# Kernel tuning notes

Hardware: AMD Instinct MI355X
Metric: run time of the kernel (lower is better)

The kernel has to match this reference:

```python
import jax, jax.numpy as jnp
import numpy as np
from jax import lax

L = 8
PATCH = 3
DIRS = [(0, 1), (1, 0), (1, 1), (1, -1)]


def _pair_indices():
    coords = np.arange(PATCH * PATCH)
    rr, cc = coords // PATCH, coords % PATCH
    i1s, i2s = [], []
    for dr, dc in DIRS:
        m = (rr + dr >= 0) & (rr + dr < PATCH) & (cc + dc >= 0) & (cc + dc < PATCH)
        i1s.append(coords[m])
        i2s.append((rr[m] + dr) * PATCH + (cc[m] + dc))
    return np.concatenate(i1s), np.concatenate(i2s)

_I1, _I2 = _pair_indices()


def conv_bn_silu(x, w, s, b, pad):
    # Conv2d(bias=False) + eval-mode BatchNorm folded into (s, b) + SiLU
    y = lax.conv_general_dilated(x, w, (1, 1), [(pad, pad), (pad, pad)],
                                 dimension_numbers=("NCHW", "OIHW", "NCHW"))
    y = y * s[None, :, None, None] + b[None, :, None, None]
    return jax.nn.silu(y)


def glcm_feats(x):
    B, C, H, W = x.shape
    pad = PATCH // 2
    xp = jnp.pad(x, ((0, 0), (0, 0), (pad, pad), (pad, pad)), mode="edge")
    # unfold: (B, C, 9, H, W)
    patches = jnp.stack([xp[:, :, i:i + H, j:j + W]
                         for i in range(PATCH) for j in range(PATCH)], axis=2)
    q = jnp.clip((patches * (L - 1)).astype(jnp.int32), 0, L - 1)
    q = q.reshape(B * C, PATCH * PATCH, H * W)
    # co-occurrence pair indices for all 4 directions, concatenated: (BC, K, HW)
    idx = q[:, _I1, :] * L + q[:, _I2, :]
    idx = idx.transpose(0, 2, 1)  # (BC, HW, K)
    # per-pixel local histogram over L*L bins (scatter-add)
    hist = jax.vmap(jax.vmap(
        lambda v: jnp.zeros((L * L,), x.dtype).at[v].add(1.0)))(idx)
    hist = hist / len(DIRS)  # reduce_mode='average'
    s = jnp.maximum(hist.sum(-1, keepdims=True), 1e-6)
    p = hist / s  # (BC, HW, L*L)
    li = jnp.arange(L, dtype=x.dtype)
    diff = li[:, None] - li[None, :]
    diff_sq = (diff ** 2).reshape(-1)
    abs_d = jnp.abs(diff).reshape(-1)
    contrast = (p * diff_sq).sum(-1)
    energy = (p * p).sum(-1)
    entropy = -(p * jnp.log(p + 1e-6)).sum(-1)
    homog = (p / (1.0 + abs_d)).sum(-1)
    f = jnp.stack([contrast, energy, entropy, homog], axis=-1)  # (BC, HW, 4)
    f = f.reshape(B, C, H * W, 4).mean(axis=1)  # average over channels
    return f.transpose(0, 2, 1).reshape(B, 4, H, W)


def setup_inputs() -> dict:
    key = jax.random.key(0)
    B, C, H, W = 4, 64, 80, 80
    c_, cb, c2 = 32, 16, 64
    ks = iter(jax.random.split(key, 20))
    x = jax.random.uniform(next(ks), (B, C, H, W), jnp.float32)

    def conv_p(cin, cout, ksz):
        w = jax.random.normal(next(ks), (cout, cin, ksz, ksz), jnp.float32) / np.sqrt(cin * ksz * ksz)
        s = jax.random.uniform(next(ks), (cout,), jnp.float32, 0.5, 1.5)
        b = jax.random.normal(next(ks), (cout,), jnp.float32) * 0.1
        return w, s, b

    cv1_w, cv1_s, cv1_b = conv_p(C + 4, c_, 1)
    cv2_w, cv2_s, cv2_b = conv_p(C + 4, c_, 1)
    m1_w, m1_s, m1_b = conv_p(c_, cb, 1)
    m2_w, m2_s, m2_b = conv_p(cb, c_, 3)
    cv3_w, cv3_s, cv3_b = conv_p(2 * c_, c2, 1)
    return dict(x=x, cv1_w=cv1_w, cv1_s=cv1_s, cv1_b=cv1_b,
                cv2_w=cv2_w, cv2_s=cv2_s, cv2_b=cv2_b,
                m1_w=m1_w, m1_s=m1_s, m1_b=m1_b,
                m2_w=m2_w, m2_s=m2_s, m2_b=m2_b,
                cv3_w=cv3_w, cv3_s=cv3_s, cv3_b=cv3_b)


def reference(x, cv1_w, cv1_s, cv1_b, cv2_w, cv2_s, cv2_b,
              m1_w, m1_s, m1_b, m2_w, m2_s, m2_b,
              cv3_w, cv3_s, cv3_b):
    g = glcm_feats(x)
    xc = jnp.concatenate([x, g], axis=1)  # (B, C+4, H, W)
    a = conv_bn_silu(xc, cv1_w, cv1_s, cv1_b, 0)
    y = conv_bn_silu(a, m1_w, m1_s, m1_b, 0)
    y = conv_bn_silu(y, m2_w, m2_s, m2_b, 1)
    a = a + y  # Bottleneck shortcut (c1 == c2)
    b = conv_bn_silu(xc, cv2_w, cv2_s, cv2_b, 0)
    return conv_bn_silu(jnp.concatenate([a, b], axis=1), cv3_w, cv3_s, cv3_b, 0)
```

## Files before the change

### kernel.cpp

```cpp
#include <hip/hip_runtime.h>
#include <math.h>

constexpr int B = 4, C = 64, H = 80, W = 80;
constexpr int HW = H * W;
constexpr int NPIX = B * HW;

static __device__ __forceinline__ float silu(float v) {
    float e = __expf(-v);
    return v * __builtin_amdgcn_rcpf(1.0f + e);
}

static __device__ __forceinline__ void ce(unsigned &x, unsigned &y) {
    unsigned mn, mx;
    asm("v_pk_min_u16 %0, %2, %3\n\t"
        "v_pk_max_u16 %1, %2, %3"
        : "=&v"(mn), "=v"(mx) : "v"(x), "v"(y));
    x = mn; y = mx;
}

__global__ __launch_bounds__(256) void glcm_kernel(const float* __restrict__ x,
                                                   float* __restrict__ g) {
    const int t = threadIdx.x;
    const int pxl = t & 7;
    const int grp = t >> 3;
    const int pix = blockIdx.x * 8 + pxl;
    const int b = pix / HW;
    const int hw = pix - b * HW;
    const int h = hw / W;
    const int w = hw - h * W;
    const int hm = h > 0 ? h - 1 : 0;
    const int hp = h < H - 1 ? h + 1 : H - 1;
    const int wm = w > 0 ? w - 1 : 0;
    const int wp = w < W - 1 ? w + 1 : W - 1;
    const int o[9] = {hm * W + wm, hm * W + w, hm * W + wp,
                      h  * W + wm, h  * W + w, h  * W + wp,
                      hp * W + wm, hp * W + w, hp * W + wp};
    const float* c0 = x + (size_t)(b * C + grp * 2) * HW;
    const float* c1 = c0 + HW;

    int q0[9], q1[9];
    #pragma unroll
    for (int k = 0; k < 9; ++k) {
        int a0 = (int)(c0[o[k]] * 7.0f);
        int a1 = (int)(c1[o[k]] * 7.0f);
        a0 = a0 < 0 ? 0 : a0; q0[k] = a0 > 7 ? 7 : a0;
        a1 = a1 < 0 ? 0 : a1; q1[k] = a1 > 7 ? 7 : a1;
    }

    static constexpr int PA[20] = {0,1,3,4,6,7, 0,1,2,3,4,5, 0,1,3,4, 1,2,4,5};
    static constexpr int PB[20] = {1,2,4,5,7,8, 3,4,5,6,7,8, 4,5,7,8, 3,4,6,7};

    int csum = 0;
    float hsum = 0.f;
    unsigned key[20];
    #pragma unroll
    for (int a = 0; a < 20; ++a) {
        const int d0 = q0[PA[a]] - q0[PB[a]];
        const int d1 = q1[PA[a]] - q1[PB[a]];
        csum += d0 * d0 + d1 * d1;
        const int a0 = d0 < 0 ? -d0 : d0;
        const int a1 = d1 < 0 ? -d1 : d1;
        hsum += __builtin_amdgcn_rcpf((float)(1 + a0))
              + __builtin_amdgcn_rcpf((float)(1 + a1));
        key[a] = (unsigned)((q0[PA[a]] * 8 + q0[PB[a]])
                          | ((q1[PA[a]] * 8 + q1[PB[a]]) << 16));
    }

    #pragma unroll
    for (int p = 1; p < 32; p <<= 1) {
        #pragma unroll
        for (int k = p; k >= 1; k >>= 1) {
            const int jm = k % p;
            #pragma unroll
            for (int lo = 0; lo < 20; ++lo) {
                const int hi = lo + k;
                if (hi < 20 && lo >= jm && ((lo - jm) % (2 * k)) < k &&
                    (lo / (2 * p)) == (hi / (2 * p))) {
                    ce(key[lo], key[hi]);
                }
            }
        }
    }

    float psum = 0.f, lsum = 0.f;
    #pragma unroll
    for (int hh = 0; hh < 2; ++hh) {
        const int sh = hh * 16;
        float p_[20];
        float pc = 0.f;
        p_[0] = 0.f;
        unsigned prev = (key[0] >> sh) & 0xFFFFu;
        #pragma unroll
        for (int a = 1; a < 20; ++a) {
            const unsigned cur = (key[a] >> sh) & 0xFFFFu;
            pc = (cur == prev) ? pc + 1.f : 0.f;
            p_[a] = pc;
            psum += pc;
            prev = cur;
        }
        float r = 0.f;
        float prod = p_[19] + 1.f;
        prev = (key[19] >> sh) & 0xFFFFu;
        #pragma unroll
        for (int a = 18; a >= 0; --a) {
            const unsigned cur = (key[a] >> sh) & 0xFFFFu;
            r = (cur == prev) ? r + 1.f : 0.f;
            prod *= (p_[a] + r + 1.f);
            prev = cur;
        }
        lsum += __logf(prod);
    }

    float fc = (float)csum * (1.f / 20.f);
    float fe = (psum * 2.f + 40.f) * (1.f / 400.f);
    float fn = -(lsum + 40.f * -2.9957322736f ) * (1.f / 20.f);
    float fh = hsum * (1.f / 20.f);

    #pragma unroll
    for (int m = 8; m < 64; m <<= 1) {
        fc += __shfl_xor(fc, m);
        fe += __shfl_xor(fe, m);
        fn += __shfl_xor(fn, m);
        fh += __shfl_xor(fh, m);
    }
    __shared__ float red[4][8][4];
    const int wv = t >> 6;
    if ((t & 63) < 8) {
        red[wv][pxl][0] = fc; red[wv][pxl][1] = fe;
        red[wv][pxl][2] = fn; red[wv][pxl][3] = fh;
    }
    __syncthreads();
    if (t < 32) {
        const int p2 = t >> 2, f = t & 3;
        float s = red[0][p2][f] + red[1][p2][f] + red[2][p2][f] + red[3][p2][f];
        s *= (1.f / 64.f);
        const int pix2 = blockIdx.x * 8 + p2;
        const int b2 = pix2 / HW;
        const int hw2 = pix2 - b2 * HW;
        g[((size_t)(b2 * 4 + f)) * HW + hw2] = s;
    }
}

__global__ __launch_bounds__(512) void stage1_kernel(
    const float* __restrict__ x, const float* __restrict__ g,
    const float* __restrict__ w1, const float* __restrict__ s1, const float* __restrict__ b1,
    const float* __restrict__ w2, const float* __restrict__ s2, const float* __restrict__ b2,
    const float* __restrict__ wm1, const float* __restrict__ sm1, const float* __restrict__ bm1,
    float* __restrict__ a, float* __restrict__ bbuf, float* __restrict__ y16) {
    __shared__ float aT[32][64];
    const int t = threadIdx.x;
    const int lane = t & 63;
    const int wv = __builtin_amdgcn_readfirstlane(t >> 6);
    const int oc0 = wv * 4;
    const int pix = blockIdx.x * 64 + lane;
    const int bi = pix / HW;
    const int hw = pix - bi * HW;
    const float* xp = x + (size_t)(bi * C) * HW + hw;
    const float* gp = g + (size_t)(bi * 4) * HW + hw;

    float acc1[4] = {0.f, 0.f, 0.f, 0.f};
    float acc2[4] = {0.f, 0.f, 0.f, 0.f};
    #pragma unroll 8
    for (int ic = 0; ic < C; ++ic) {
        const float xv = xp[(size_t)ic * HW];
        #pragma unroll
        for (int j = 0; j < 4; ++j) {
            acc1[j] += xv * w1[(oc0 + j) * 68 + ic];
            acc2[j] += xv * w2[(oc0 + j) * 68 + ic];
        }
    }
    #pragma unroll
    for (int ic = 0; ic < 4; ++ic) {
        const float gv = gp[(size_t)ic * HW];
        #pragma unroll
        for (int j = 0; j < 4; ++j) {
            acc1[j] += gv * w1[(oc0 + j) * 68 + 64 + ic];
            acc2[j] += gv * w2[(oc0 + j) * 68 + 64 + ic];
        }
    }
    #pragma unroll
    for (int j = 0; j < 4; ++j) {
        const int oc = oc0 + j;
        const float v1 = silu(acc1[j] * s1[oc] + b1[oc]);
        a[((size_t)(bi * 32 + oc)) * HW + hw] = v1;
        aT[oc][lane] = v1;
        bbuf[((size_t)(bi * 32 + oc)) * HW + hw] = silu(acc2[j] * s2[oc] + b2[oc]);
    }
    __syncthreads();
    const int om0 = wv * 2;
    float accm[2] = {0.f, 0.f};
    #pragma unroll 8
    for (int ic = 0; ic < 32; ++ic) {
        const float av = aT[ic][lane];
        #pragma unroll
        for (int j = 0; j < 2; ++j) accm[j] += av * wm1[(om0 + j) * 32 + ic];
    }
    #pragma unroll
    for (int j = 0; j < 2; ++j) {
        const int oc = om0 + j;
        y16[((size_t)(bi * 16 + oc)) * HW + hw] = silu(accm[j] * sm1[oc] + bm1[oc]);
    }
}

__global__ __launch_bounds__(512) void m2cv3_kernel(
    const float* __restrict__ y16, const float* __restrict__ a,
    const float* __restrict__ bbuf,
    const float* __restrict__ wm2, const float* __restrict__ sm2, const float* __restrict__ bm2,
    const float* __restrict__ wc, const float* __restrict__ sc, const float* __restrict__ bc,
    float* __restrict__ out) {
    __shared__ float a2[32][64];
    const int t = threadIdx.x;
    const int lane = t & 63;
    const int wv = __builtin_amdgcn_readfirstlane(t >> 6);
    const int oc0 = wv * 4;
    const int pix = blockIdx.x * 64 + lane;
    const int bi = pix / HW;
    const int hw = pix - bi * HW;
    const int h = hw / W;
    const int w = hw - h * W;
    const float* yp = y16 + (size_t)(bi * 16) * HW;

    float acc[4] = {0.f, 0.f, 0.f, 0.f};
    for (int ic = 0; ic < 16; ++ic) {
        #pragma unroll
        for (int kh = 0; kh < 3; ++kh) {
            const int rr = h + kh - 1;
            const bool rin = (rr >= 0) && (rr < H);
            #pragma unroll
            for (int kw = 0; kw < 3; ++kw) {
                const int cc = w + kw - 1;
                const bool in = rin && (cc >= 0) && (cc < W);
                const float yv = in ? yp[(size_t)ic * HW + rr * W + cc] : 0.0f;
                #pragma unroll
                for (int j = 0; j < 4; ++j)
                    acc[j] += yv * wm2[(((oc0 + j) * 16 + ic) * 3 + kh) * 3 + kw];
            }
        }
    }
    #pragma unroll
    for (int j = 0; j < 4; ++j) {
        const int oc = oc0 + j;
        const float v = a[((size_t)(bi * 32 + oc)) * HW + hw]
                      + silu(acc[j] * sm2[oc] + bm2[oc]);
        a2[oc][lane] = v;
    }
    __syncthreads();
    const int oc3 = wv * 8;
    const float* bp = bbuf + (size_t)(bi * 32) * HW + hw;
    float acc3[8];
    #pragma unroll
    for (int j = 0; j < 8; ++j) acc3[j] = 0.f;
    #pragma unroll 8
    for (int ic = 0; ic < 32; ++ic) {
        const float av = a2[ic][lane];
        #pragma unroll
        for (int j = 0; j < 8; ++j) acc3[j] += av * wc[(oc3 + j) * 64 + ic];
    }
    #pragma unroll 8
    for (int ic = 0; ic < 32; ++ic) {
        const float bv = bp[(size_t)ic * HW];
        #pragma unroll
        for (int j = 0; j < 8; ++j) acc3[j] += bv * wc[(oc3 + j) * 64 + 32 + ic];
    }
    #pragma unroll
    for (int j = 0; j < 8; ++j) {
        const int oc = oc3 + j;
        out[((size_t)(bi * 64 + oc)) * HW + hw] = silu(acc3[j] * sc[oc] + bc[oc]);
    }
}

extern "C" void kernel_launch(void* const* d_in, const int* in_sizes, int n_in,
                              void* d_out, int out_size, void* d_ws, size_t ws_size,
                              hipStream_t stream) {
    const float* x    = (const float*)d_in[0];
    const float* cv1w = (const float*)d_in[1];
    const float* cv1s = (const float*)d_in[2];
    const float* cv1b = (const float*)d_in[3];
    const float* cv2w = (const float*)d_in[4];
    const float* cv2s = (const float*)d_in[5];
    const float* cv2b = (const float*)d_in[6];
    const float* m1w  = (const float*)d_in[7];
    const float* m1s  = (const float*)d_in[8];
    const float* m1b  = (const float*)d_in[9];
    const float* m2w  = (const float*)d_in[10];
    const float* m2s  = (const float*)d_in[11];
    const float* m2b  = (const float*)d_in[12];
    const float* cv3w = (const float*)d_in[13];
    const float* cv3s = (const float*)d_in[14];
    const float* cv3b = (const float*)d_in[15];

    float* ws   = (float*)d_ws;
    float* g    = ws;
    float* a    = ws + 102400;
    float* bbuf = ws + 921600;
    float* y16  = ws + 1740800;

    glcm_kernel<<<NPIX / 8, 256, 0, stream>>>(x, g);
    stage1_kernel<<<NPIX / 64, 512, 0, stream>>>(x, g, cv1w, cv1s, cv1b,
                                                 cv2w, cv2s, cv2b,
                                                 m1w, m1s, m1b, a, bbuf, y16);
    m2cv3_kernel<<<NPIX / 64, 512, 0, stream>>>(y16, a, bbuf, m2w, m2s, m2b,
                                                cv3w, cv3s, cv3b, (float*)d_out);
}
```

Baseline: 64.75 us.

## Use packed FP32 FMA with pre-paired weights and packed u16 GLCM math

Adds a small kernel that interleaves pairs of output-channel weights into 64-bit words, so the 1x1 and 3x3 conv loops can use v_pk_fma_f32 with a scalar-register weight pair, halving FMA instruction count. The GLCM kernel is reworked to keep both channels' quantized values packed in 16-bit lanes and compute differences, keys, run lengths and products with packed u16 ops, replacing the per-half scalar loops. This adds an extra kernel launch each call and relies on inline asm with SGPR operands for weights.

```diff
diff --git a/kernel.cpp b/kernel.cpp
--- a/kernel.cpp
+++ b/kernel.cpp
@@ -5,17 +5,49 @@
 constexpr int HW = H * W;
 constexpr int NPIX = B * HW;
 
+typedef float f32x2 __attribute__((ext_vector_type(2)));
+typedef unsigned u32;
+typedef unsigned long long u64;
+
 static __device__ __forceinline__ float silu(float v) {
     float e = __expf(-v);
     return v * __builtin_amdgcn_rcpf(1.0f + e);
 }
 
-static __device__ __forceinline__ void ce(unsigned &x, unsigned &y) {
-    unsigned mn, mx;
+static __device__ __forceinline__ u32 pks(u32 a, u32 b){u32 d; asm("v_pk_sub_u16 %0,%1,%2":"=v"(d):"v"(a),"v"(b)); return d;}
+static __device__ __forceinline__ u32 pka(u32 a, u32 b){u32 d; asm("v_pk_add_u16 %0,%1,%2":"=v"(d):"v"(a),"v"(b)); return d;}
+static __device__ __forceinline__ u32 pkm(u32 a, u32 b){u32 d; asm("v_pk_mul_lo_u16 %0,%1,%2":"=v"(d):"v"(a),"v"(b)); return d;}
+static __device__ __forceinline__ u32 pkmin(u32 a, u32 b){u32 d; asm("v_pk_min_u16 %0,%1,%2":"=v"(d):"v"(a),"v"(b)); return d;}
+static __device__ __forceinline__ u32 pkmaxi(u32 a, u32 b){u32 d; asm("v_pk_max_i16 %0,%1,%2":"=v"(d):"v"(a),"v"(b)); return d;}
+static __device__ __forceinline__ float cb0(u32 a){float f; asm("v_cvt_f32_ubyte0 %0,%1":"=v"(f):"v"(a)); return f;}
+static __device__ __forceinline__ float cb2(u32 a){float f; asm("v_cvt_f32_ubyte2 %0,%1":"=v"(f):"v"(a)); return f;}
+
+static __device__ __forceinline__ void ce(u32 &x, u32 &y) {
+    u32 mn, mx;
     asm("v_pk_min_u16 %0, %2, %3\n\t"
         "v_pk_max_u16 %1, %2, %3"
         : "=&v"(mn), "=v"(mx) : "v"(x), "v"(y));
     x = mn; y = mx;
+}
+
+static __device__ __forceinline__ void pkfma(f32x2 &acc, f32x2 a, u64 w){
+    asm("v_pk_fma_f32 %0, %1, %2, %0" : "+v"(acc) : "v"(a), "s"(w));
+}
+
+__global__ __launch_bounds__(256) void pack_weights(
+    const float* __restrict__ w1, const float* __restrict__ w2,
+    const float* __restrict__ wm2, const float* __restrict__ wc,
+    u64* __restrict__ wp1, u64* __restrict__ wp2,
+    u64* __restrict__ wpm2, u64* __restrict__ wpc) {
+    const int i = blockIdx.x * 256 + threadIdx.x;
+    auto pack2 = [](const float* w, int p, int L, int j) -> u64 {
+        return ((u64)__float_as_uint(w[(2*p+1)*L + j]) << 32)
+             | (u64)__float_as_uint(w[2*p*L + j]);
+    };
+    if (i < 1088)      wp1[i] = pack2(w1, i / 68, 68, i % 68);
+    else if (i < 2176) { int k = i - 1088; wp2[k]  = pack2(w2,  k / 68,  68,  k % 68); }
+    else if (i < 4480) { int k = i - 2176; wpm2[k] = pack2(wm2, k / 144, 144, k % 144); }
+    else if (i < 6528) { int k = i - 4480; wpc[k]  = pack2(wc,  k / 64,  64,  k % 64); }
 }
 
 __global__ __launch_bounds__(256) void glcm_kernel(const float* __restrict__ x,
@@ -38,32 +70,32 @@
     const float* c0 = x + (size_t)(b * C + grp * 2) * HW;
     const float* c1 = c0 + HW;
 
-    int q0[9], q1[9];
+    u32 qpk[9];
     #pragma unroll
     for (int k = 0; k < 9; ++k) {
         int a0 = (int)(c0[o[k]] * 7.0f);
         int a1 = (int)(c1[o[k]] * 7.0f);
-        a0 = a0 < 0 ? 0 : a0; q0[k] = a0 > 7 ? 7 : a0;
-        a1 = a1 < 0 ? 0 : a1; q1[k] = a1 > 7 ? 7 : a1;
+        a0 = a0 < 0 ? 0 : (a0 > 7 ? 7 : a0);
+        a1 = a1 < 0 ? 0 : (a1 > 7 ? 7 : a1);
+        qpk[k] = (u32)a0 | ((u32)a1 << 16);
     }
 
     static constexpr int PA[20] = {0,1,3,4,6,7, 0,1,2,3,4,5, 0,1,3,4, 1,2,4,5};
     static constexpr int PB[20] = {1,2,4,5,7,8, 3,4,5,6,7,8, 4,5,7,8, 3,4,6,7};
 
-    int csum = 0;
+    const u32 ONEpk = 0x00010001u, EIGHTpk = 0x00080008u;
+    u32 cs = 0;
     float hsum = 0.f;
-    unsigned key[20];
+    u32 key[20];
     #pragma unroll
     for (int a = 0; a < 20; ++a) {
-        const int d0 = q0[PA[a]] - q0[PB[a]];
-        const int d1 = q1[PA[a]] - q1[PB[a]];
-        csum += d0 * d0 + d1 * d1;
-        const int a0 = d0 < 0 ? -d0 : d0;
-        const int a1 = d1 < 0 ? -d1 : d1;
-        hsum += __builtin_amdgcn_rcpf((float)(1 + a0))
-              + __builtin_amdgcn_rcpf((float)(1 + a1));
-        key[a] = (unsigned)((q0[PA[a]] * 8 + q0[PB[a]])
-                          | ((q1[PA[a]] * 8 + q1[PB[a]]) << 16));
+        const u32 qa = qpk[PA[a]], qb = qpk[PB[a]];
+        const u32 d = pks(qa, qb);
+        cs = pka(cs, pkm(d, d));
+        const u32 ad = pkmaxi(d, pks(0u, d));
+        const u32 h1 = pka(ad, ONEpk);
+        hsum += __builtin_amdgcn_rcpf(cb0(h1)) + __builtin_amdgcn_rcpf(cb2(h1));
+        key[a] = pka(pkm(qa, EIGHTpk), qb);
     }
 
     #pragma unroll
@@ -82,37 +114,38 @@
         }
     }
 
-    float psum = 0.f, lsum = 0.f;
-    #pragma unroll
-    for (int hh = 0; hh < 2; ++hh) {
-        const int sh = hh * 16;
-        float p_[20];
-        float pc = 0.f;
-        p_[0] = 0.f;
-        unsigned prev = (key[0] >> sh) & 0xFFFFu;
-        #pragma unroll
-        for (int a = 1; a < 20; ++a) {
-            const unsigned cur = (key[a] >> sh) & 0xFFFFu;
-            pc = (cur == prev) ? pc + 1.f : 0.f;
-            p_[a] = pc;
-            psum += pc;
-            prev = cur;
-        }
-        float r = 0.f;
-        float prod = p_[19] + 1.f;
-        prev = (key[19] >> sh) & 0xFFFFu;
-        #pragma unroll
-        for (int a = 18; a >= 0; --a) {
-            const unsigned cur = (key[a] >> sh) & 0xFFFFu;
-            r = (cur == prev) ? r + 1.f : 0.f;
-            prod *= (p_[a] + r + 1.f);
-            prev = cur;
-        }
-        lsum += __logf(prod);
-    }
+    u32 eq[20];
+    #pragma unroll
+    for (int a = 1; a < 20; ++a)
+        eq[a] = pks(ONEpk, pkmin(pks(key[a], key[a - 1]), ONEpk));
+
+    u32 pc = 0, ps = 0, pv[20];
+    pv[0] = 0;
+    #pragma unroll
+    for (int a = 1; a < 20; ++a) {
+        pc = pkm(pka(pc, ONEpk), eq[a]);
+        pv[a] = pc;
+        ps = pka(ps, pc);
+    }
+    float pr0, pr1;
+    {
+        const u32 m = pka(pv[19], ONEpk);
+        pr0 = cb0(m); pr1 = cb2(m);
+    }
+    u32 rc = 0;
+    #pragma unroll
+    for (int a = 18; a >= 0; --a) {
+        rc = pkm(pka(rc, ONEpk), eq[a + 1]);
+        const u32 m = pka(pka(pv[a], rc), ONEpk);
+        pr0 *= cb0(m); pr1 *= cb2(m);
+    }
+
+    const int csum = (int)(cs & 0xFFFFu) + (int)(cs >> 16);
+    const int psum = (int)(ps & 0xFFFFu) + (int)(ps >> 16);
+    const float lsum = __logf(pr0) + __logf(pr1);
 
     float fc = (float)csum * (1.f / 20.f);
-    float fe = (psum * 2.f + 40.f) * (1.f / 400.f);
+    float fe = ((float)psum * 2.f + 40.f) * (1.f / 400.f);
     float fn = -(lsum + 40.f * -2.9957322736f ) * (1.f / 20.f);
     float fh = hsum * (1.f / 20.f);
 
@@ -143,8 +176,8 @@
 
 __global__ __launch_bounds__(512) void stage1_kernel(
     const float* __restrict__ x, const float* __restrict__ g,
-    const float* __restrict__ w1, const float* __restrict__ s1, const float* __restrict__ b1,
-    const float* __restrict__ w2, const float* __restrict__ s2, const float* __restrict__ b2,
+    const u64* __restrict__ wp1, const float* __restrict__ s1, const float* __restrict__ b1,
+    const u64* __restrict__ wp2, const float* __restrict__ s2, const float* __restrict__ b2,
     const float* __restrict__ wm1, const float* __restrict__ sm1, const float* __restrict__ bm1,
     float* __restrict__ a, float* __restrict__ bbuf, float* __restrict__ y16) {
     __shared__ float aT[32][64];
@@ -152,39 +185,43 @@
     const int lane = t & 63;
     const int wv = __builtin_amdgcn_readfirstlane(t >> 6);
     const int oc0 = wv * 4;
+    const int p0 = wv * 2;
     const int pix = blockIdx.x * 64 + lane;
     const int bi = pix / HW;
     const int hw = pix - bi * HW;
     const float* xp = x + (size_t)(bi * C) * HW + hw;
     const float* gp = g + (size_t)(bi * 4) * HW + hw;
 
-    float acc1[4] = {0.f, 0.f, 0.f, 0.f};
-    float acc2[4] = {0.f, 0.f, 0.f, 0.f};
+    f32x2 acc1[2] = {{0.f, 0.f}, {0.f, 0.f}};
+    f32x2 acc2[2] = {{0.f, 0.f}, {0.f, 0.f}};
     #pragma unroll 8
     for (int ic = 0; ic < C; ++ic) {
         const float xv = xp[(size_t)ic * HW];
-        #pragma unroll
-        for (int j = 0; j < 4; ++j) {
-            acc1[j] += xv * w1[(oc0 + j) * 68 + ic];
-            acc2[j] += xv * w2[(oc0 + j) * 68 + ic];
-        }
+        const f32x2 av = {xv, xv};
+        pkfma(acc1[0], av, wp1[(p0    ) * 68 + ic]);
+        pkfma(acc1[1], av, wp1[(p0 + 1) * 68 + ic]);
+        pkfma(acc2[0], av, wp2[(p0    ) * 68 + ic]);
+        pkfma(acc2[1], av, wp2[(p0 + 1) * 68 + ic]);
     }
     #pragma unroll
     for (int ic = 0; ic < 4; ++ic) {
         const float gv = gp[(size_t)ic * HW];
-        #pragma unroll
-        for (int j = 0; j < 4; ++j) {
-            acc1[j] += gv * w1[(oc0 + j) * 68 + 64 + ic];
-            acc2[j] += gv * w2[(oc0 + j) * 68 + 64 + ic];
-        }
-    }
-    #pragma unroll
-    for (int j = 0; j < 4; ++j) {
-        const int oc = oc0 + j;
-        const float v1 = silu(acc1[j] * s1[oc] + b1[oc]);
-        a[((size_t)(bi * 32 + oc)) * HW + hw] = v1;
-        aT[oc][lane] = v1;
-        bbuf[((size_t)(bi * 32 + oc)) * HW + hw] = silu(acc2[j] * s2[oc] + b2[oc]);
+        const f32x2 av = {gv, gv};
+        pkfma(acc1[0], av, wp1[(p0    ) * 68 + 64 + ic]);
+        pkfma(acc1[1], av, wp1[(p0 + 1) * 68 + 64 + ic]);
+        pkfma(acc2[0], av, wp2[(p0    ) * 68 + 64 + ic]);
+        pkfma(acc2[1], av, wp2[(p0 + 1) * 68 + 64 + ic]);
+    }
+    #pragma unroll
+    for (int j = 0; j < 2; ++j) {
+        #pragma unroll
+        for (int hf = 0; hf < 2; ++hf) {
+            const int oc = oc0 + j * 2 + hf;
+            const float v1 = silu(acc1[j][hf] * s1[oc] + b1[oc]);
+            a[((size_t)(bi * 32 + oc)) * HW + hw] = v1;
+            aT[oc][lane] = v1;
+            bbuf[((size_t)(bi * 32 + oc)) * HW + hw] = silu(acc2[j][hf] * s2[oc] + b2[oc]);
+        }
     }
     __syncthreads();
     const int om0 = wv * 2;
@@ -205,14 +242,15 @@
 __global__ __launch_bounds__(512) void m2cv3_kernel(
     const float* __restrict__ y16, const float* __restrict__ a,
     const float* __restrict__ bbuf,
-    const float* __restrict__ wm2, const float* __restrict__ sm2, const float* __restrict__ bm2,
-    const float* __restrict__ wc, const float* __restrict__ sc, const float* __restrict__ bc,
+    const u64* __restrict__ wpm2, const float* __restrict__ sm2, const float* __restrict__ bm2,
+    const u64* __restrict__ wpc, const float* __restrict__ sc, const float* __restrict__ bc,
     float* __restrict__ out) {
     __shared__ float a2[32][64];
     const int t = threadIdx.x;
     const int lane = t & 63;
     const int wv = __builtin_amdgcn_readfirstlane(t >> 6);
     const int oc0 = wv * 4;
+    const int pm0 = wv * 2;
     const int pix = blockIdx.x * 64 + lane;
     const int bi = pix / HW;
     const int hw = pix - bi * HW;
@@ -220,7 +258,7 @@
     const int w = hw - h * W;
     const float* yp = y16 + (size_t)(bi * 16) * HW;
 
-    float acc[4] = {0.f, 0.f, 0.f, 0.f};
+    f32x2 accm[2] = {{0.f, 0.f}, {0.f, 0.f}};
     for (int ic = 0; ic < 16; ++ic) {
         #pragma unroll
         for (int kh = 0; kh < 3; ++kh) {
@@ -231,41 +269,51 @@
                 const int cc = w + kw - 1;
                 const bool in = rin && (cc >= 0) && (cc < W);
                 const float yv = in ? yp[(size_t)ic * HW + rr * W + cc] : 0.0f;
-                #pragma unroll
-                for (int j = 0; j < 4; ++j)
-                    acc[j] += yv * wm2[(((oc0 + j) * 16 + ic) * 3 + kh) * 3 + kw];
+                const f32x2 yv2 = {yv, yv};
+                const int j9 = ic * 9 + kh * 3 + kw;
+                pkfma(accm[0], yv2, wpm2[(pm0    ) * 144 + j9]);
+                pkfma(accm[1], yv2, wpm2[(pm0 + 1) * 144 + j9]);
             }
         }
     }
     #pragma unroll
-    for (int j = 0; j < 4; ++j) {
-        const int oc = oc0 + j;
-        const float v = a[((size_t)(bi * 32 + oc)) * HW + hw]
-                      + silu(acc[j] * sm2[oc] + bm2[oc]);
-        a2[oc][lane] = v;
+    for (int j = 0; j < 2; ++j) {
+        #pragma unroll
+        for (int hf = 0; hf < 2; ++hf) {
+            const int oc = oc0 + j * 2 + hf;
+            const float v = a[((size_t)(bi * 32 + oc)) * HW + hw]
+                          + silu(accm[j][hf] * sm2[oc] + bm2[oc]);
+            a2[oc][lane] = v;
+        }
     }
     __syncthreads();
     const int oc3 = wv * 8;
+    const int pc0 = wv * 4;
     const float* bp = bbuf + (size_t)(bi * 32) * HW + hw;
-    float acc3[8];
-    #pragma unroll
-    for (int j = 0; j < 8; ++j) acc3[j] = 0.f;
+    f32x2 acc3[4] = {{0.f, 0.f}, {0.f, 0.f}, {0.f, 0.f}, {0.f, 0.f}};
     #pragma unroll 8
     for (int ic = 0; ic < 32; ++ic) {
         const float av = a2[ic][lane];
-        #pragma unroll
-        for (int j = 0; j < 8; ++j) acc3[j] += av * wc[(oc3 + j) * 64 + ic];
+        const f32x2 av2 = {av, av};
+        #pragma unroll
+        for (int j = 0; j < 4; ++j)
+            pkfma(acc3[j], av2, wpc[(pc0 + j) * 64 + ic]);
     }
     #pragma unroll 8
     for (int ic = 0; ic < 32; ++ic) {
         const float bv = bp[(size_t)ic * HW];
-        #pragma unroll
-        for (int j = 0; j < 8; ++j) acc3[j] += bv * wc[(oc3 + j) * 64 + 32 + ic];
-    }
-    #pragma unroll
-    for (int j = 0; j < 8; ++j) {
-        const int oc = oc3 + j;
-        out[((size_t)(bi * 64 + oc)) * HW + hw] = silu(acc3[j] * sc[oc] + bc[oc]);
+        const f32x2 bv2 = {bv, bv};
+        #pragma unroll
+        for (int j = 0; j < 4; ++j)
+            pkfma(acc3[j], bv2, wpc[(pc0 + j) * 64 + 32 + ic]);
+    }
+    #pragma unroll
+    for (int j = 0; j < 4; ++j) {
+        #pragma unroll
+        for (int hf = 0; hf < 2; ++hf) {
+            const int oc = oc3 + j * 2 + hf;
+            out[((size_t)(bi * 64 + oc)) * HW + hw] = silu(acc3[j][hf] * sc[oc] + bc[oc]);
+        }
     }
 }
 
@@ -294,11 +342,18 @@
     float* a    = ws + 102400;
     float* bbuf = ws + 921600;
     float* y16  = ws + 1740800;
-
+    u64* wpbase = (u64*)(ws + 2150400);
+    u64* wp1  = wpbase;
+    u64* wp2  = wpbase + 1088;
+    u64* wpm2 = wpbase + 2176;
+    u64* wpc  = wpbase + 4480;
+
+    pack_weights<<<26, 256, 0, stream>>>(cv1w, cv2w, m2w, cv3w,
+                                         wp1, wp2, wpm2, wpc);
     glcm_kernel<<<NPIX / 8, 256, 0, stream>>>(x, g);
-    stage1_kernel<<<NPIX / 64, 512, 0, stream>>>(x, g, cv1w, cv1s, cv1b,
-                                                 cv2w, cv2s, cv2b,
+    stage1_kernel<<<NPIX / 64, 512, 0, stream>>>(x, g, wp1, cv1s, cv1b,
+                                                 wp2, cv2s, cv2b,
                                                  m1w, m1s, m1b, a, bbuf, y16);
-    m2cv3_kernel<<<NPIX / 64, 512, 0, stream>>>(y16, a, bbuf, m2w, m2s, m2b,
-                                                cv3w, cv3s, cv3b, (float*)d_out);
-}
+    m2cv3_kernel<<<NPIX / 64, 512, 0, stream>>>(y16, a, bbuf, wpm2, m2s, m2b,
+                                                wpc, cv3s, cv3b, (float*)d_out);
+}
```

Result: slower. 80.97 us (+25.1%).
